# Kernel tuning notes

Measured on AMD Instinct MI355X. Metric: run time of the kernel, lower is better.

The kernel has to match this reference:

```python
import jax, jax.numpy as jnp
import numpy as np
from jax import lax
import math

KS = 7  # attention kernel size
PAD = 3


def conv2d(x, w, b, pad):
    y = lax.conv_general_dilated(x, w, (1, 1), [(pad, pad), (pad, pad)],
                                 dimension_numbers=('NCHW', 'OIHW', 'NCHW'))
    return y + b[None, :, None, None]


def unfold(x):
    # x: [B, C, H, W] -> [B, C, KS*KS, H, W], matching nn.Unfold channel-major order
    B, C, H, W = x.shape
    xp = jnp.pad(x, ((0, 0), (0, 0), (PAD, PAD), (PAD, PAD)))
    patches = [xp[:, :, i:i + H, j:j + W] for i in range(KS) for j in range(KS)]
    return jnp.stack(patches, axis=2)


def setup_inputs() -> dict:
    key = jax.random.key(0)
    ks = jax.random.split(key, 12)
    B, H, W = 1, 256, 256
    s = lambda fan: 1.0 / np.sqrt(fan)
    inp = {
        'x': jax.random.normal(ks[0], (B, 6, H, W), jnp.float32),
        'w0': jax.random.normal(ks[1], (48, 3, 3, 3), jnp.float32) * s(3 * 9),
        'b0': jnp.zeros((48,), jnp.float32),
        'w1': jax.random.normal(ks[2], (48, 48, 3, 3), jnp.float32) * s(48 * 9),
        'b1': jnp.zeros((48,), jnp.float32),
        'w2': jax.random.normal(ks[3], (48, 48, 3, 3), jnp.float32) * s(48 * 9),
        'b2': jnp.zeros((48,), jnp.float32),
        'w3': jax.random.normal(ks[4], (24, 48, 3, 3), jnp.float32) * s(48 * 9),
        'b3': jnp.zeros((24,), jnp.float32),
        'skip_w': jax.random.normal(ks[5], (24, 3, 1, 1), jnp.float32) * s(3),
        'skip_b': jnp.zeros((24,), jnp.float32),
        'q_w': jax.random.normal(ks[6], (24, 24, 1, 1), jnp.float32) * s(24),
        'q_b': jnp.zeros((24,), jnp.float32),
        'k_w': jax.random.normal(ks[7], (24, 24, 1, 1), jnp.float32) * s(24),
        'k_b': jnp.zeros((24,), jnp.float32),
        'v_w': jax.random.normal(ks[8], (24, 24, 1, 1), jnp.float32) * s(24),
        'v_b': jnp.zeros((24,), jnp.float32),
    }
    return inp


def reference(x, w0, b0, w1, b1, w2, b2, w3, b3, skip_w, skip_b,
              q_w, q_b, k_w, k_b, v_w, v_b):
    def submodel(t):
        h = jax.nn.relu(conv2d(t, w0, b0, 1))
        h = jax.nn.relu(conv2d(h, w1, b1, 1))
        h = jax.nn.relu(conv2d(h, w2, b2, 1))
        h = jax.nn.relu(conv2d(h, w3, b3, 1))
        return h + conv2d(t, skip_w, skip_b, 0)

    xa, xb = jnp.split(x, 2, axis=1)  # [B,3,H,W] each
    a = submodel(xa)                  # [B,24,H,W]
    b = submodel(xb)

    Q = conv2d(b, q_w, q_b, 0)        # [B,24,H,W]
    K = unfold(conv2d(a, k_w, k_b, 0))  # [B,24,49,H,W]
    V = unfold(conv2d(a, v_w, v_b, 0))  # [B,24,49,H,W]

    C = Q.shape[1]
    A = jnp.einsum('bchw,bcphw->bphw', Q, K) / math.sqrt(C)
    A = jax.nn.softmax(A, axis=1)     # softmax over 49 local positions
    y = jnp.einsum('bphw,bcphw->bchw', A, V)
    return jnp.concatenate([y + a, b], axis=1)  # [B,48,H,W]
```

## Files before the change

### kernel.cpp

```cpp
#include <hip/hip_runtime.h>
#include <math.h>

#define HH 256
#define WW 256
#define NN (HH * WW)

typedef _Float16 f16;
typedef _Float16 f16x4 __attribute__((ext_vector_type(4)));
typedef _Float16 f16x8 __attribute__((ext_vector_type(8)));
typedef float f32x4 __attribute__((ext_vector_type(4)));

#define OQ 75264
#define CS 48
#define IS 36

__device__ inline float dot8p(f16x8 a, f16x8 b, float acc) {
#if __has_builtin(__builtin_amdgcn_fdot2)
  acc = __builtin_amdgcn_fdot2(__builtin_shufflevector(a, a, 0, 1),
                               __builtin_shufflevector(b, b, 0, 1), acc, false);
  acc = __builtin_amdgcn_fdot2(__builtin_shufflevector(a, a, 2, 3),
                               __builtin_shufflevector(b, b, 2, 3), acc, false);
  acc = __builtin_amdgcn_fdot2(__builtin_shufflevector(a, a, 4, 5),
                               __builtin_shufflevector(b, b, 4, 5), acc, false);
  acc = __builtin_amdgcn_fdot2(__builtin_shufflevector(a, a, 6, 7),
                               __builtin_shufflevector(b, b, 6, 7), acc, false);
  return acc;
#else
#pragma unroll
  for (int i = 0; i < 8; ++i) acc += (float)a[i] * (float)b[i];
  return acc;
#endif
}

__device__ __forceinline__ float repack_elem(
    int e, const float* __restrict__ w0, const float* __restrict__ w1,
    const float* __restrict__ w2, const float* __restrict__ w3,
    const float* __restrict__ qw, const float* __restrict__ kw,
    const float* __restrict__ vw) {
  const int O1 = 1536, O2 = O1 + 27648, O3 = O2 + 27648;
  float val = 0.f;
  if (e >= OQ) {
    int idx = e - OQ;
    int mat = idx >> 10;
    int r = idx & 1023;
    int nt = r >> 9;
    int ln = (r >> 3) & 63;
    int j = r & 7;
    int nn = ln & 15, qd = ln >> 4;
    int ci = qd * 8 + j, co = nt * 16 + nn;
    const float* w = (mat == 0) ? qw : (mat == 1) ? kw : vw;
    if (ci < 24 && co < 24) val = w[co * 24 + ci];
  } else if (e < O1) {
    int j = e & 7;
    int ln = (e >> 3) & 63;
    int nt = e >> 9;
    int nn = ln & 15, qd = ln >> 4;
    int k = qd * 8 + j;
    int cout = nt * 16 + nn;
    if (k < 27) {
      int tap = k / 3, ci = k - tap * 3;
      val = w0[(cout * 3 + ci) * 9 + tap];
    }
  } else {
    const float* w;
    int COUT, idx;
    if (e < O2)      { w = w1; COUT = 48; idx = e - O1; }
    else if (e < O3) { w = w2; COUT = 48; idx = e - O2; }
    else             { w = w3; COUT = 24; idx = e - O3; }
    const int NT = (COUT == 48) ? 3 : 2;
    int j = idx & 7;
    int ln = (idx >> 3) & 63;
    int rest = idx >> 9;
    int nt = rest % NT;
    int q2 = rest / NT;
    int kc = q2 & 1;
    int tap = q2 >> 1;
    int nn = ln & 15, qd = ln >> 4;
    int ci = kc * 32 + qd * 8 + j;
    int cout = nt * 16 + nn;
    if (ci < 48 && cout < COUT) val = w[(cout * 48 + ci) * 9 + tap];
  }
  return val;
}

__global__ __launch_bounds__(256) void prep(
    const float* __restrict__ w0, const float* __restrict__ w1,
    const float* __restrict__ w2, const float* __restrict__ w3,
    const float* __restrict__ qw, const float* __restrict__ kw,
    const float* __restrict__ vw, f16* __restrict__ bf) {
  int e = blockIdx.x * 256 + threadIdx.x;
  bf[e] = (f16)repack_elem(e, w0, w1, w2, w3, qw, kw, vw);
}

template <int W_IN, int W_OUT, int H_OUT, int MAXT>
__device__ __forceinline__ void stage_mid(const f16* __restrict__ inb,
                                          f16* __restrict__ outb,
                                          const f16* __restrict__ bfr,
                                          const float* __restrict__ bias,
                                          int gy0, int gx0, int tid) {
  const int P = W_OUT * H_OUT;
  const int T = (P + 15) >> 4;
  const int lane = tid & 63, wave = tid >> 6;
  const int n = lane & 15, quad = lane >> 4;
  const int cbase = quad * 4;
  f32x4 acc[MAXT][3];
  int ay[MAXT], ax[MAXT];
  float4 bv[3];
#pragma unroll
  for (int nt = 0; nt < 3; ++nt)
    bv[nt] = *(const float4*)(bias + nt * 16 + cbase);
#pragma unroll
  for (int ti = 0; ti < MAXT; ++ti) {
    int qa = (wave + 4 * ti) * 16 + n;
    int qc = (qa > P - 1) ? (P - 1) : qa;
    ay[ti] = qc / W_OUT;
    ax[ti] = qc - ay[ti] * W_OUT;
#pragma unroll
    for (int nt = 0; nt < 3; ++nt)
      acc[ti][nt] = (f32x4){bv[nt].x, bv[nt].y, bv[nt].z, bv[nt].w};
  }
#pragma unroll 1
  for (int tap = 0; tap < 9; ++tap) {
    const int dy = tap / 3, dx = tap - dy * 3;
    f16x8 B[2][3];
#pragma unroll
    for (int kc = 0; kc < 2; ++kc)
#pragma unroll
      for (int nt = 0; nt < 3; ++nt)
        B[kc][nt] =
            *(const f16x8*)(bfr + (((tap * 2 + kc) * 3 + nt) * 64 + lane) * 8);
#pragma unroll
    for (int ti = 0; ti < MAXT; ++ti) {
      if (wave + 4 * ti < T) {
        const f16* ap = inb + ((ay[ti] + dy) * W_IN + ax[ti] + dx) * CS +
                        quad * 8;
        f16x8 a0 = *(const f16x8*)(ap);
        f16x8 a1 = *(const f16x8*)(ap + 32);
#pragma unroll
        for (int nt = 0; nt < 3; ++nt)
          acc[ti][nt] = __builtin_amdgcn_mfma_f32_16x16x32_f16(
              B[0][nt], a0, acc[ti][nt], 0, 0, 0);
#pragma unroll
        for (int nt = 0; nt < 3; ++nt)
          acc[ti][nt] = __builtin_amdgcn_mfma_f32_16x16x32_f16(
              B[1][nt], a1, acc[ti][nt], 0, 0, 0);
      }
    }
  }
#pragma unroll
  for (int ti = 0; ti < MAXT; ++ti) {
    int qa = (wave + 4 * ti) * 16 + n;
    if (wave + 4 * ti < T && qa < P) {
      int gy = gy0 + ay[ti], gx = gx0 + ax[ti];
      bool im = (gy >= 0 && gy < HH && gx >= 0 && gx < WW);
#pragma unroll
      for (int nt = 0; nt < 3; ++nt) {
        f16x4 h;
#pragma unroll
        for (int reg = 0; reg < 4; ++reg)
          h[reg] = (f16)(im ? fmaxf(acc[ti][nt][reg], 0.f) : 0.f);
        *(f16x4*)(outb + qa * CS + nt * 16 + cbase) = h;
      }
    }
  }
}

__global__ __launch_bounds__(256, 3) void fused_conv(
    const float* __restrict__ x, const float* __restrict__ b0,
    const float* __restrict__ b1, const float* __restrict__ b2,
    const float* __restrict__ b3, const float* __restrict__ sw,
    const float* __restrict__ sb, f16* __restrict__ ABh,
    const f16* __restrict__ BF) {
  extern __shared__ char smem[];
  f16* bufA = (f16*)smem;
  f16* bufB = (f16*)(smem + 29568);
  const int tid = threadIdx.x;
  const int bz = blockIdx.x;
  const int z = bz >> 9, tt = bz & 511;
  const int bx = (tt & 15) * 16, by = (tt >> 4) * 8;
  const int lane = tid & 63, wave = tid >> 6;
  const int n = lane & 15, quad = lane >> 4;
  const int cbase = quad * 4;
  const float* xz = x + (size_t)z * 3 * NN;

  for (int i = tid; i < 3292; i += 256) {
    f16x8 zz = {};
    *(f16x8*)(smem + i * 16) = zz;
  }
  __syncthreads();

  for (int p = tid; p < 308; p += 256) {
    int py = p / 22, px = p - py * 22;
    int gy = by - 3 + py, gx = bx - 3 + px;
    f16* row = bufB + p * IS;
#pragma unroll
    for (int tap = 0; tap < 9; ++tap) {
      int dy = tap / 3, dx = tap - (tap / 3) * 3;
      int sy = gy + dy - 1, sx = gx + dx - 1;
      f16 c0 = (f16)0.f, c1 = c0, c2 = c0;
      if (sy >= 0 && sy < HH && sx >= 0 && sx < WW) {
        int o = sy * WW + sx;
        c0 = (f16)xz[o];
        c1 = (f16)xz[NN + o];
        c2 = (f16)xz[2 * NN + o];
      }
      row[tap * 3 + 0] = c0;
      row[tap * 3 + 1] = c1;
      row[tap * 3 + 2] = c2;
    }
#pragma unroll
    for (int k = 27; k < 32; ++k) row[k] = (f16)0.f;
  }
  __syncthreads();

  {
    f16x8 B0[3];
#pragma unroll
    for (int nt = 0; nt < 3; ++nt)
      B0[nt] = *(const f16x8*)(BF + (nt * 64 + lane) * 8);
    float4 bv[3];
#pragma unroll
    for (int nt = 0; nt < 3; ++nt)
      bv[nt] = *(const float4*)(b0 + nt * 16 + cbase);
    f32x4 acc[5][3];
    int pya[5], pxa[5];
#pragma unroll
    for (int ti = 0; ti < 5; ++ti) {
      int qa = (wave + 4 * ti) * 16 + n;
      int qc = (qa > 307) ? 307 : qa;
      pya[ti] = qc / 22;
      pxa[ti] = qc - pya[ti] * 22;
#pragma unroll
      for (int nt = 0; nt < 3; ++nt)
        acc[ti][nt] = (f32x4){bv[nt].x, bv[nt].y, bv[nt].z, bv[nt].w};
    }
#pragma unroll
    for (int ti = 0; ti < 5; ++ti) {
      int qa = (wave + 4 * ti) * 16 + n;
      int qc = (qa > 307) ? 307 : qa;
      f16x8 a = *(const f16x8*)(bufB + qc * IS + quad * 8);
#pragma unroll
      for (int nt = 0; nt < 3; ++nt)
        acc[ti][nt] = __builtin_amdgcn_mfma_f32_16x16x32_f16(B0[nt], a,
                                                             acc[ti][nt], 0,
                                                             0, 0);
    }
    __syncthreads();
#pragma unroll
    for (int ti = 0; ti < 5; ++ti) {
      int qa = (wave + 4 * ti) * 16 + n;
      if (qa < 308) {
        int gy = by - 3 + pya[ti], gx = bx - 3 + pxa[ti];
        bool im = (gy >= 0 && gy < HH && gx >= 0 && gx < WW);
#pragma unroll
        for (int nt = 0; nt < 3; ++nt) {
          f16x4 h;
#pragma unroll
          for (int reg = 0; reg < 4; ++reg)
            h[reg] = (f16)(im ? fmaxf(acc[ti][nt][reg], 0.f) : 0.f);
          *(f16x4*)(bufA + qa * CS + nt * 16 + cbase) = h;
        }
      }
    }
  }
  __syncthreads();

  stage_mid<22, 20, 12, 4>(bufA, bufB, BF + 1536, b1, by - 2, bx - 2, tid);
  __syncthreads();
  stage_mid<20, 18, 10, 3>(bufB, bufA, BF + 29184, b2, by - 1, bx - 1, tid);
  __syncthreads();

  {
    f32x4 acc[2][2];
    int ay[2], ax[2];
    float skw0[2][4], skw1[2][4], skw2[2][4], skb4[2][4];
#pragma unroll
    for (int nt = 0; nt < 2; ++nt)
#pragma unroll
      for (int reg = 0; reg < 4; ++reg) {
        int cc = nt * 16 + cbase + reg;
        bool v = (cc < 24);
        skw0[nt][reg] = v ? sw[cc * 3 + 0] : 0.f;
        skw1[nt][reg] = v ? sw[cc * 3 + 1] : 0.f;
        skw2[nt][reg] = v ? sw[cc * 3 + 2] : 0.f;
        skb4[nt][reg] = v ? sb[cc] : 0.f;
      }
#pragma unroll
    for (int ti = 0; ti < 2; ++ti) {
      int qa = (wave + 4 * ti) * 16 + n;
      ay[ti] = qa >> 4;
      ax[ti] = qa & 15;
#pragma unroll
      for (int nt = 0; nt < 2; ++nt) {
        int cc0 = nt * 16 + cbase;
        float4 bv = (cc0 < 24) ? *(const float4*)(b3 + cc0)
                               : make_float4(0.f, 0.f, 0.f, 0.f);
        acc[ti][nt] = (f32x4){bv.x, bv.y, bv.z, bv.w};
      }
    }
#pragma unroll 1
    for (int tap = 0; tap < 9; ++tap) {
      const int dy = tap / 3, dx = tap - dy * 3;
      f16x8 B[2][2];
#pragma unroll
      for (int kc = 0; kc < 2; ++kc)
#pragma unroll
        for (int nt = 0; nt < 2; ++nt)
          B[kc][nt] = *(const f16x8*)(BF + 56832 +
                                      (((tap * 2 + kc) * 2 + nt) * 64 + lane) *
                                          8);
#pragma unroll
      for (int ti = 0; ti < 2; ++ti) {
        const f16* ap = bufA + ((ay[ti] + dy) * 18 + ax[ti] + dx) * CS +
                        quad * 8;
        f16x8 a0 = *(const f16x8*)(ap);
        f16x8 a1 = *(const f16x8*)(ap + 32);
#pragma unroll
        for (int nt = 0; nt < 2; ++nt)
          acc[ti][nt] = __builtin_amdgcn_mfma_f32_16x16x32_f16(
              B[0][nt], a0, acc[ti][nt], 0, 0, 0);
#pragma unroll
        for (int nt = 0; nt < 2; ++nt)
          acc[ti][nt] = __builtin_amdgcn_mfma_f32_16x16x32_f16(
              B[1][nt], a1, acc[ti][nt], 0, 0, 0);
      }
    }
    f16* oz = ABh + (size_t)z * NN * 32;
#pragma unroll
    for (int ti = 0; ti < 2; ++ti) {
      int o = (by + ay[ti]) * WW + bx + ax[ti];
      float xv0 = xz[o], xv1 = xz[NN + o], xv2 = xz[2 * NN + o];
#pragma unroll
      for (int nt = 0; nt < 2; ++nt) {
        int cc0 = nt * 16 + cbase;
        if (cc0 < 24) {
          f16x4 h;
#pragma unroll
          for (int reg = 0; reg < 4; ++reg) {
            float sk = skb4[nt][reg] + skw0[nt][reg] * xv0 +
                       skw1[nt][reg] * xv1 + skw2[nt][reg] * xv2;
            h[reg] = (f16)(fmaxf(acc[ti][nt][reg], 0.f) + sk);
          }
          *(f16x4*)(oz + (size_t)o * 32 + cc0) = h;
        }
      }
    }
#pragma unroll
    for (int ti = 0; ti < 2; ++ti) {
      int o = (by + ay[ti]) * WW + bx + ax[ti];
      if (quad >= 2) {
        f16x4 zz = {};
        *(f16x4*)(oz + (size_t)o * 32 + 16 + cbase) = zz;
      }
    }
  }
}

__global__ __launch_bounds__(256, 3) void attn_q(
    const f16* __restrict__ ABh, const f16* __restrict__ BF,
    const float* __restrict__ qw, const float* __restrict__ qb,
    const float* __restrict__ kb, const float* __restrict__ vb,
    float* __restrict__ out) {
  extern __shared__ char smem[];
  f16* kv = (f16*)smem;
  f16* Wq = (f16*)(smem + 35840);
  float* Qbv = (float*)(smem + 35840 + 1152);
  const int tid = threadIdx.x;
  const int lane = tid & 63, wave = tid >> 6;
  const int n = lane & 15, quad = lane >> 4;
  const int cbase = quad * 4;
  const int bxA = ((int)blockIdx.x & 15) * 16, byA = ((int)blockIdx.x >> 4) * 8;

  for (int i = tid; i < 576; i += 256) Wq[i] = (f16)qw[i];
  if (tid < 24) Qbv[tid] = qb[tid];

  for (int idx = tid; idx < 1232; idx += 256) {
    int slot = idx >> 2, c = idx & 3;
    int row = slot / 22, pxl = slot - row * 22;
    int gy = byA + row - 3, gx = bxA + pxl - 3;
    f16x8 v = {};
    if (gy >= 0 && gy < HH && gx >= 0 && gx < WW)
      v = *(const f16x8*)(ABh + ((size_t)(gy * WW + gx)) * 32 + c * 8);
    *(f16x8*)(kv + slot * 56 + c * 8) = v;
  }
  __syncthreads();

  const int t7 = tid & 127, half = tid >> 7;
  const int yl = t7 >> 4, xl = t7 & 15;
  const int pg = (byA + yl) * WW + bxA + xl;

  const f16* cs = kv + ((yl + 3) * 22 + (xl + 3)) * 56;
  f16x8 a0 = *(const f16x8*)(cs);
  f16x8 a1 = *(const f16x8*)(cs + 8);
  f16x8 a2 = *(const f16x8*)(cs + 16);

  const f16* bhp = ABh + (size_t)NN * 32 + (size_t)pg * 32;
  f16x8 bb0 = *(const f16x8*)(bhp);
  f16x8 bb1 = *(const f16x8*)(bhp + 8);
  f16x8 bb2 = *(const f16x8*)(bhp + 16);
  float qf[24];
#pragma unroll
  for (int co = 0; co < 24; ++co) {
    float acc = Qbv[co];
    acc = dot8p(bb0, *(const f16x8*)(Wq + co * 24), acc);
    acc = dot8p(bb1, *(const f16x8*)(Wq + co * 24 + 8), acc);
    acc = dot8p(bb2, *(const f16x8*)(Wq + co * 24 + 16), acc);
    qf[co] = acc;
  }
  f16x8 q0, q1, q2;
#pragma unroll
  for (int c = 0; c < 8; ++c) {
    q0[c] = (f16)qf[c];
    q1[c] = (f16)qf[8 + c];
    q2[c] = (f16)qf[16 + c];
  }
  __syncthreads();

  {
    f16x8 KF[2], VF[2];
#pragma unroll
    for (int nt = 0; nt < 2; ++nt) {
      KF[nt] = *(const f16x8*)(BF + OQ + 1024 + (nt * 64 + lane) * 8);
      VF[nt] = *(const f16x8*)(BF + OQ + 2048 + (nt * 64 + lane) * 8);
    }
    float4 kb4[2], vb4[2];
#pragma unroll
    for (int nt = 0; nt < 2; ++nt) {
      int cc0 = nt * 16 + cbase;
      kb4[nt] = (cc0 < 24) ? *(const float4*)(kb + cc0)
                           : make_float4(0.f, 0.f, 0.f, 0.f);
      vb4[nt] = (cc0 < 24) ? *(const float4*)(vb + cc0)
                           : make_float4(0.f, 0.f, 0.f, 0.f);
    }
    for (int t = wave; t < 20; t += 4) {
      f16x8 a8 = *(const f16x8*)(kv + (t * 16 + n) * 56 + quad * 8);
      f16x4 hk[2], hv[2];
#pragma unroll
      for (int nt = 0; nt < 2; ++nt) {
        f32x4 ak = {kb4[nt].x, kb4[nt].y, kb4[nt].z, kb4[nt].w};
        f32x4 av = {vb4[nt].x, vb4[nt].y, vb4[nt].z, vb4[nt].w};
        ak = __builtin_amdgcn_mfma_f32_16x16x32_f16(KF[nt], a8, ak, 0, 0, 0);
        av = __builtin_amdgcn_mfma_f32_16x16x32_f16(VF[nt], a8, av, 0, 0, 0);
#pragma unroll
        for (int reg = 0; reg < 4; ++reg) {
          hk[nt][reg] = (f16)ak[reg];
          hv[nt][reg] = (f16)av[reg];
        }
      }
      f16* slot = kv + (t * 16 + n) * 56;
#pragma unroll
      for (int nt = 0; nt < 2; ++nt) {
        int cc0 = nt * 16 + cbase;
        if (cc0 < 24) {
          *(f16x4*)(slot + cc0) = hk[nt];
          *(f16x4*)(slot + 24 + cc0) = hv[nt];
        }
      }
    }
  }
  __syncthreads();

  float s[25];
  float m = -3e38f;
#pragma unroll
  for (int i = 0; i < 25; ++i) {
    int pp = half * 25 + i;
    if (pp < 49) {
      int dy = pp / 7, dx = pp - (pp / 7) * 7;
      const f16* base = kv + ((yl + dy) * 22 + (xl + dx)) * 56;
      f16x8 k0 = *(const f16x8*)(base);
      f16x8 k1 = *(const f16x8*)(base + 8);
      f16x8 k2 = *(const f16x8*)(base + 16);
      float d = 0.f;
      d = dot8p(q0, k0, d);
      d = dot8p(q1, k1, d);
      d = dot8p(q2, k2, d);
      s[i] = d * 0.20412414523193154f;
      m = fmaxf(m, s[i]);
    } else {
      s[i] = -3e38f;
    }
  }
  float den = 0.f;
#pragma unroll
  for (int i = 0; i < 25; ++i) {
    float e = __expf(s[i] - m);
    s[i] = e;
    den += e;
  }

  f16x8 y0 = {}, y1 = {}, y2 = {};
#pragma unroll
  for (int i = 0; i < 25; ++i) {
    int pp = half * 25 + i;
    if (pp < 49) {
      int dy = pp / 7, dx = pp - (pp / 7) * 7;
      const f16* base = kv + ((yl + dy) * 22 + (xl + dx)) * 56 + 24;
      f16 wh = (f16)s[i];
      f16x8 w8 = {wh, wh, wh, wh, wh, wh, wh, wh};
      f16x8 v0 = *(const f16x8*)(base);
      f16x8 v1 = *(const f16x8*)(base + 8);
      f16x8 v2 = *(const f16x8*)(base + 16);
      y0 = v0 * w8 + y0;
      y1 = v1 * w8 + y1;
      y2 = v2 * w8 + y2;
    }
  }
  __syncthreads();

  if (half == 1) {
    f16* ex = kv + t7 * 56;
    *(f16x8*)(ex) = y0;
    *(f16x8*)(ex + 8) = y1;
    *(f16x8*)(ex + 16) = y2;
    float* mf = (float*)(ex + 24);
    mf[0] = m;
    mf[1] = den;
  }
  __syncthreads();

  if (half == 0) {
    const f16* ex = kv + t7 * 56;
    f16x8 yb0 = *(const f16x8*)(ex);
    f16x8 yb1 = *(const f16x8*)(ex + 8);
    f16x8 yb2 = *(const f16x8*)(ex + 16);
    const float* mf = (const float*)(ex + 24);
    float mB = mf[0], dB = mf[1];
    float M = fmaxf(m, mB);
    float fa = __expf(m - M), fb = __expf(mB - M);
    float inv = 1.f / (den * fa + dB * fb);
#pragma unroll
    for (int c = 0; c < 8; ++c) {
      out[(size_t)c * NN + pg] =
          ((float)y0[c] * fa + (float)yb0[c] * fb) * inv + (float)a0[c];
      out[(size_t)(8 + c) * NN + pg] =
          ((float)y1[c] * fa + (float)yb1[c] * fb) * inv + (float)a1[c];
      out[(size_t)(16 + c) * NN + pg] =
          ((float)y2[c] * fa + (float)yb2[c] * fb) * inv + (float)a2[c];
    }
  } else {
#pragma unroll
    for (int c = 0; c < 8; ++c) {
      out[(size_t)(24 + c) * NN + pg] = (float)bb0[c];
      out[(size_t)(32 + c) * NN + pg] = (float)bb1[c];
      out[(size_t)(40 + c) * NN + pg] = (float)bb2[c];
    }
  }
}

extern "C" void kernel_launch(void* const* d_in, const int* in_sizes, int n_in,
                              void* d_out, int out_size, void* d_ws,
                              size_t ws_size, hipStream_t stream) {
  const float* x = (const float*)d_in[0];
  const float* w0 = (const float*)d_in[1];
  const float* b0 = (const float*)d_in[2];
  const float* w1 = (const float*)d_in[3];
  const float* b1 = (const float*)d_in[4];
  const float* w2 = (const float*)d_in[5];
  const float* b2 = (const float*)d_in[6];
  const float* w3 = (const float*)d_in[7];
  const float* b3 = (const float*)d_in[8];
  const float* sw = (const float*)d_in[9];
  const float* sb = (const float*)d_in[10];
  const float* qw = (const float*)d_in[11];
  const float* qb = (const float*)d_in[12];
  const float* kw = (const float*)d_in[13];
  const float* kb = (const float*)d_in[14];
  const float* vw = (const float*)d_in[15];
  const float* vb = (const float*)d_in[16];
  float* out = (float*)d_out;

  f16* base = (f16*)d_ws;
  f16* ABh = base;
  f16* BF = base + (size_t)64 * NN;

  prep<<<dim3(306), dim3(256), 0, stream>>>(w0, w1, w2, w3, qw, kw, vw, BF);
  fused_conv<<<dim3(1024), dim3(256), 52672, stream>>>(x, b0, b1, b2, b3, sw,
                                                       sb, ABh, BF);
  attn_q<<<dim3(512), dim3(256), 37088, stream>>>(ABh, BF, qw, qb, kb, vb,
                                                  out);
}
```

Measured before the change: 151.8 us.

## Prefetch next-tap weights, pad LDS channel stride, lower occupancy bound

Register double-buffers the per-tap MFMA weight fragments in the mid conv stages and the final conv stage, so the next tap's global load overlaps the current tap's MFMAs. It also pads the LDS channel strides (48→56, 36→40) to cut bank conflicts, and hoists the first-layer weight load ahead of the LDS zeroing. Launch bounds drop from 3 to 2 blocks per CU to give the extra registers room, and shared memory per block grows to 61440 bytes. The risk is lower occupancy, which may expose latency elsewhere.

```diff
diff --git a/kernel.cpp b/kernel.cpp
--- a/kernel.cpp
+++ b/kernel.cpp
@@ -11,8 +11,8 @@
 typedef float f32x4 __attribute__((ext_vector_type(4)));
 
 #define OQ 75264
-#define CS 48
-#define IS 36
+#define CS 56
+#define IS 40
 
 __device__ inline float dot8p(f16x8 a, f16x8 b, float acc) {
 #if __has_builtin(__builtin_amdgcn_fdot2)
@@ -105,6 +105,14 @@
   const int cbase = quad * 4;
   f32x4 acc[MAXT][3];
   int ay[MAXT], ax[MAXT];
+
+  f16x8 Bc[2][3];
+#pragma unroll
+  for (int kc = 0; kc < 2; ++kc)
+#pragma unroll
+    for (int nt = 0; nt < 3; ++nt)
+      Bc[kc][nt] = *(const f16x8*)(bfr + ((kc * 3 + nt) * 64 + lane) * 8);
+
   float4 bv[3];
 #pragma unroll
   for (int nt = 0; nt < 3; ++nt)
@@ -122,13 +130,17 @@
 #pragma unroll 1
   for (int tap = 0; tap < 9; ++tap) {
     const int dy = tap / 3, dx = tap - dy * 3;
-    f16x8 B[2][3];
-#pragma unroll
-    for (int kc = 0; kc < 2; ++kc)
-#pragma unroll
-      for (int nt = 0; nt < 3; ++nt)
-        B[kc][nt] =
-            *(const f16x8*)(bfr + (((tap * 2 + kc) * 3 + nt) * 64 + lane) * 8);
+    f16x8 Bn[2][3];
+    if (tap < 8) {
+#pragma unroll
+      for (int kc = 0; kc < 2; ++kc)
+#pragma unroll
+        for (int nt = 0; nt < 3; ++nt)
+          Bn[kc][nt] = *(const f16x8*)(bfr + ((((tap + 1) * 2 + kc) * 3 + nt) *
+                                                  64 +
+                                              lane) *
+                                                 8);
+    }
 #pragma unroll
     for (int ti = 0; ti < MAXT; ++ti) {
       if (wave + 4 * ti < T) {
@@ -139,12 +151,18 @@
 #pragma unroll
         for (int nt = 0; nt < 3; ++nt)
           acc[ti][nt] = __builtin_amdgcn_mfma_f32_16x16x32_f16(
-              B[0][nt], a0, acc[ti][nt], 0, 0, 0);
+              Bc[0][nt], a0, acc[ti][nt], 0, 0, 0);
 #pragma unroll
         for (int nt = 0; nt < 3; ++nt)
           acc[ti][nt] = __builtin_amdgcn_mfma_f32_16x16x32_f16(
-              B[1][nt], a1, acc[ti][nt], 0, 0, 0);
-      }
+              Bc[1][nt], a1, acc[ti][nt], 0, 0, 0);
+      }
+    }
+    if (tap < 8) {
+#pragma unroll
+      for (int kc = 0; kc < 2; ++kc)
+#pragma unroll
+        for (int nt = 0; nt < 3; ++nt) Bc[kc][nt] = Bn[kc][nt];
     }
   }
 #pragma unroll
@@ -165,7 +183,7 @@
   }
 }
 
-__global__ __launch_bounds__(256, 3) void fused_conv(
+__global__ __launch_bounds__(256, 2) void fused_conv(
     const float* __restrict__ x, const float* __restrict__ b0,
     const float* __restrict__ b1, const float* __restrict__ b2,
     const float* __restrict__ b3, const float* __restrict__ sw,
@@ -173,7 +191,7 @@
     const f16* __restrict__ BF) {
   extern __shared__ char smem[];
   f16* bufA = (f16*)smem;
-  f16* bufB = (f16*)(smem + 29568);
+  f16* bufB = (f16*)(smem + 34496);
   const int tid = threadIdx.x;
   const int bz = blockIdx.x;
   const int z = bz >> 9, tt = bz & 511;
@@ -183,7 +201,12 @@
   const int cbase = quad * 4;
   const float* xz = x + (size_t)z * 3 * NN;
 
-  for (int i = tid; i < 3292; i += 256) {
+  f16x8 B0[3];
+#pragma unroll
+  for (int nt = 0; nt < 3; ++nt)
+    B0[nt] = *(const f16x8*)(BF + (nt * 64 + lane) * 8);
+
+  for (int i = tid; i < 3840; i += 256) {
     f16x8 zz = {};
     *(f16x8*)(smem + i * 16) = zz;
   }
@@ -214,10 +237,6 @@
   __syncthreads();
 
   {
-    f16x8 B0[3];
-#pragma unroll
-    for (int nt = 0; nt < 3; ++nt)
-      B0[nt] = *(const f16x8*)(BF + (nt * 64 + lane) * 8);
     float4 bv[3];
 #pragma unroll
     for (int nt = 0; nt < 3; ++nt)
@@ -273,6 +292,13 @@
   {
     f32x4 acc[2][2];
     int ay[2], ax[2];
+    f16x8 Bc[2][2];
+#pragma unroll
+    for (int kc = 0; kc < 2; ++kc)
+#pragma unroll
+      for (int nt = 0; nt < 2; ++nt)
+        Bc[kc][nt] =
+            *(const f16x8*)(BF + 56832 + ((kc * 2 + nt) * 64 + lane) * 8);
     float skw0[2][4], skw1[2][4], skw2[2][4], skb4[2][4];
 #pragma unroll
     for (int nt = 0; nt < 2; ++nt)
@@ -301,14 +327,17 @@
 #pragma unroll 1
     for (int tap = 0; tap < 9; ++tap) {
       const int dy = tap / 3, dx = tap - dy * 3;
-      f16x8 B[2][2];
-#pragma unroll
-      for (int kc = 0; kc < 2; ++kc)
-#pragma unroll
-        for (int nt = 0; nt < 2; ++nt)
-          B[kc][nt] = *(const f16x8*)(BF + 56832 +
-                                      (((tap * 2 + kc) * 2 + nt) * 64 + lane) *
-                                          8);
+      f16x8 Bn[2][2];
+      if (tap < 8) {
+#pragma unroll
+        for (int kc = 0; kc < 2; ++kc)
+#pragma unroll
+          for (int nt = 0; nt < 2; ++nt)
+            Bn[kc][nt] = *(const f16x8*)(BF + 56832 +
+                                         ((((tap + 1) * 2 + kc) * 2 + nt) * 64 +
+                                          lane) *
+                                             8);
+      }
 #pragma unroll
       for (int ti = 0; ti < 2; ++ti) {
         const f16* ap = bufA + ((ay[ti] + dy) * 18 + ax[ti] + dx) * CS +
@@ -318,11 +347,17 @@
 #pragma unroll
         for (int nt = 0; nt < 2; ++nt)
           acc[ti][nt] = __builtin_amdgcn_mfma_f32_16x16x32_f16(
-              B[0][nt], a0, acc[ti][nt], 0, 0, 0);
+              Bc[0][nt], a0, acc[ti][nt], 0, 0, 0);
 #pragma unroll
         for (int nt = 0; nt < 2; ++nt)
           acc[ti][nt] = __builtin_amdgcn_mfma_f32_16x16x32_f16(
-              B[1][nt], a1, acc[ti][nt], 0, 0, 0);
+              Bc[1][nt], a1, acc[ti][nt], 0, 0, 0);
+      }
+      if (tap < 8) {
+#pragma unroll
+        for (int kc = 0; kc < 2; ++kc)
+#pragma unroll
+          for (int nt = 0; nt < 2; ++nt) Bc[kc][nt] = Bn[kc][nt];
       }
     }
     f16* oz = ABh + (size_t)z * NN * 32;
@@ -575,7 +610,7 @@
   f16* BF = base + (size_t)64 * NN;
 
   prep<<<dim3(306), dim3(256), 0, stream>>>(w0, w1, w2, w3, qw, kw, vw, BF);
-  fused_conv<<<dim3(1024), dim3(256), 52672, stream>>>(x, b0, b1, b2, b3, sw,
+  fused_conv<<<dim3(1024), dim3(256), 61440, stream>>>(x, b0, b1, b2, b3, sw,
                                                        sb, ABh, BF);
   attn_q<<<dim3(512), dim3(256), 37088, stream>>>(ABh, BF, qw, qb, kb, vb,
                                                   out);
```

Result: no change. 150.7 us (-0.7%).
